# Kernel optimization log

Measured on AMD Instinct MI355X. Metric: run time of the kernel, lower is better.

The kernel has to match this reference:

```python
import jax, jax.numpy as jnp
import numpy as np


def setup_inputs() -> dict:
    key = jax.random.key(0)
    k1, k2 = jax.random.split(key)
    d_feat, n, out_dim = 4096, 8192, 2048
    x = jax.random.normal(k1, (d_feat, n), dtype=jnp.float32)
    Psi = jax.random.normal(k2, (out_dim, n), dtype=jnp.float32)
    return {"x": x, "Psi": Psi}


def reference(x, Psi):
    # Original: out = Psi @ H @ x.T @ x with H = I_n - (1/n) * ones(n, n).
    # Psi @ H subtracts the row-mean of Psi (centering over the sample axis),
    # which is mathematically identical but avoids materializing the n x n H.
    Psi_c = Psi - jnp.mean(Psi, axis=1, keepdims=True)        # [out_dim, n]
    tmp = jnp.einsum('on,dn->od', Psi_c, x)                   # Psi_c @ x.T -> [out_dim, d]
    out = jnp.einsum('od,dn->on', tmp, x)                     # @ x -> [out_dim, n]
    return out
```

## Files before the change

### kernel.cpp

```cpp
#include <hip/hip_runtime.h>
#include <cstdint>
#include <cstddef>


typedef __bf16 bf16x8 __attribute__((ext_vector_type(8)));
typedef float f32x4 __attribute__((ext_vector_type(4)));

__device__ __forceinline__ unsigned short f2bf(float f) {
  unsigned u = __builtin_bit_cast(unsigned, f);
  u += 0x7FFFu + ((u >> 16) & 1u);
  return (unsigned short)(u >> 16);
}

__device__ __forceinline__ void gload_lds16(const void* g, void* l) {
  __builtin_amdgcn_global_load_lds(
      (const __attribute__((address_space(1))) unsigned int*)g,
      (__attribute__((address_space(3))) unsigned int*)l, 16, 0, 0);
}

__device__ __forceinline__ void barrier_nofence() {
  asm volatile("" ::: "memory");
  __builtin_amdgcn_s_barrier();
  asm volatile("" ::: "memory");
}
#define WAIT_LGKM0()                                   \
  do {                                                 \
    asm volatile("s_waitcnt lgkmcnt(0)" ::: "memory"); \
    __builtin_amdgcn_sched_barrier(0);                 \
  } while (0)
#define WAITV(N) asm volatile("s_waitcnt vmcnt(" #N ")" ::: "memory")

__global__ __launch_bounds__(512, 2) void gemm2p(
    const unsigned short* __restrict__ A, const unsigned short* __restrict__ B,
    unsigned short* __restrict__ C, int M, int Nc, int K) {
  constexpr int BM = 128, BN = 256;
  constexpr int APLANE = BM * 64, ABUF = 2 * APLANE;
  constexpr int BPLANE = BN * 64, BBUF = 2 * BPLANE;
  __shared__ __align__(1024) char lds[2 * ABUF + 2 * BBUF];
  char* Al = lds;
  char* Bl = lds + 2 * ABUF;

  const int nwg = gridDim.x * gridDim.y;
  const int wgid = blockIdx.y * gridDim.x + blockIdx.x;
  const int swz = (wgid & 7) * (nwg >> 3) + (wgid >> 3);
  const int bx = swz % gridDim.x, by = swz / gridDim.x;
  const int tileM = by * BM, tileN = bx * BN;

  const int t = threadIdx.x, lane = t & 63, wave = t >> 6;
  const int wm = wave >> 2, wn = wave & 3;
  const int rsel = lane & 15;
  const int cs = (((lane >> 4) ^ (((lane >> 3) & 1) << 1)) << 4);

  const unsigned short* Ag = A + (size_t)tileM * K;
  const unsigned short* Bg = B + (size_t)tileN * K;
  const int cgA = (((t & 3) ^ (((t >> 5) & 1) << 1))) * 8;
  const int NT = K / 64;

  auto stageA = [&](int h, int kt) {
    int b2 = kt & 1;
    int r = h * 64 + ((t >> 2) & 63);
    int kk = t >> 8;
    gload_lds16(Ag + (size_t)r * K + kt * 64 + kk * 32 + cgA,
                Al + b2 * ABUF + kk * APLANE + h * 4096 + (t & 255) * 16);
  };
  auto stageB = [&](int h, int kt) {
    int b2 = kt & 1;
#pragma unroll
    for (int kk = 0; kk < 2; ++kk) {
      int r = h * 128 + (t >> 2);
      gload_lds16(Bg + (size_t)r * K + kt * 64 + kk * 32 + cgA,
                  Bl + b2 * BBUF + kk * BPLANE + h * 8192 + t * 16);
    }
  };

  f32x4 acc[4][4] = {};
  bf16x8 aF[2][2], bFall[4][2];

  stageB(0, 0); stageA(0, 0); stageB(1, 0); stageA(1, 0);
  WAITV(1);
  barrier_nofence();

  for (int kt = 0; kt < NT; ++kt) {
    const char* Ab = Al + (kt & 1) * ABUF;
    const char* Bb = Bl + (kt & 1) * BBUF;
#pragma unroll
    for (int f = 0; f < 2; ++f)
#pragma unroll
      for (int kk = 0; kk < 2; ++kk)
        aF[f][kk] = *(const bf16x8*)(Ab + kk * APLANE +
                                     ((2 * f + wm) * 16 + rsel) * 64 + cs);
#pragma unroll
    for (int g = 0; g < 4; ++g)
#pragma unroll
      for (int kk = 0; kk < 2; ++kk)
        bFall[g][kk] = *(const bf16x8*)(Bb + kk * BPLANE +
                                        ((4 * g + wn) * 16 + rsel) * 64 + cs);
    if (kt + 1 < NT) { stageB(0, kt + 1); stageA(0, kt + 1); }
    barrier_nofence();
    WAIT_LGKM0();
    __builtin_amdgcn_s_setprio(1);
#pragma unroll
    for (int f = 0; f < 2; ++f)
#pragma unroll
      for (int g = 0; g < 4; ++g)
#pragma unroll
        for (int kk = 0; kk < 2; ++kk)
          acc[f][g] = __builtin_amdgcn_mfma_f32_16x16x32_bf16(
              aF[f][kk], bFall[g][kk], acc[f][g], 0, 0, 0);
    __builtin_amdgcn_s_setprio(0);
    if (kt == NT - 1) { WAITV(0); } else { WAITV(3); }
    barrier_nofence();
#pragma unroll
    for (int f = 0; f < 2; ++f)
#pragma unroll
      for (int kk = 0; kk < 2; ++kk)
        aF[f][kk] = *(const bf16x8*)(Ab + kk * APLANE +
                                     ((2 * (f + 2) + wm) * 16 + rsel) * 64 + cs);
    if (kt + 1 < NT) { stageB(1, kt + 1); stageA(1, kt + 1); }
    barrier_nofence();
    WAIT_LGKM0();
    __builtin_amdgcn_s_setprio(1);
#pragma unroll
    for (int f = 0; f < 2; ++f)
#pragma unroll
      for (int g = 0; g < 4; ++g)
#pragma unroll
        for (int kk = 0; kk < 2; ++kk)
          acc[2 + f][g] = __builtin_amdgcn_mfma_f32_16x16x32_bf16(
              aF[f][kk], bFall[g][kk], acc[2 + f][g], 0, 0, 0);
    __builtin_amdgcn_s_setprio(0);
    WAITV(1);
    barrier_nofence();
  }

#pragma unroll
  for (int f = 0; f < 4; ++f) {
    int row0 = tileM + (2 * f + wm) * 16 + ((lane >> 4) << 2);
#pragma unroll
    for (int g = 0; g < 4; ++g) {
      int col = tileN + (4 * g + wn) * 16 + rsel;
#pragma unroll
      for (int r = 0; r < 4; ++r)
        C[(size_t)(row0 + r) * Nc + col] = f2bf(acc[f][g][r]);
    }
  }
}

__global__ __launch_bounds__(512, 2) void gemm4p(
    const unsigned short* __restrict__ A, const unsigned short* __restrict__ B,
    float* __restrict__ C, int M, int Nc, int K) {
  constexpr int BM = 256, BN = 256;
  constexpr int APLANE = BM * 64, ABUF = 2 * APLANE;
  constexpr int BPLANE = BN * 64, BBUF = 2 * BPLANE;
  __shared__ __align__(1024) char lds[2 * ABUF + 2 * BBUF];
  char* Al = lds;
  char* Bl = lds + 2 * ABUF;

  const int nwg = gridDim.x * gridDim.y;
  const int wgid = blockIdx.y * gridDim.x + blockIdx.x;
  const int swz = (wgid & 7) * (nwg >> 3) + (wgid >> 3);
  const int bx = swz % gridDim.x, by = swz / gridDim.x;
  const int tileM = by * BM, tileN = bx * BN;

  const int t = threadIdx.x, lane = t & 63, wave = t >> 6;
  const int wm = wave >> 2, wn = wave & 3;
  const int rsel = lane & 15;
  const int cs = (((lane >> 4) ^ (((lane >> 3) & 1) << 1)) << 4);

  const unsigned short* Ag = A + (size_t)tileM * K;
  const unsigned short* Bg = B + (size_t)tileN * K;
  const int cgA = (((t & 3) ^ (((t >> 5) & 1) << 1))) * 8;
  const int NT = K / 64;

  auto stageA = [&](int h, int kt) {
    int b2 = kt & 1;
#pragma unroll
    for (int kk = 0; kk < 2; ++kk) {
      int r = h * 128 + (t >> 2);
      gload_lds16(Ag + (size_t)r * K + kt * 64 + kk * 32 + cgA,
                  Al + b2 * ABUF + kk * APLANE + h * 8192 + t * 16);
    }
  };
  auto stageB = [&](int h, int kt) {
    int b2 = kt & 1;
#pragma unroll
    for (int kk = 0; kk < 2; ++kk) {
      int r = h * 128 + (t >> 2);
      gload_lds16(Bg + (size_t)r * K + kt * 64 + kk * 32 + cgA,
                  Bl + b2 * BBUF + kk * BPLANE + h * 8192 + t * 16);
    }
  };

  f32x4 acc[8][4] = {};
  bf16x8 aF[4][2], bF0[2][2], bF1[2][2];

  stageA(0, 0); stageB(1, 0); stageA(1, 0); stageB(0, 0);
  stageA(0, 1); stageB(1, 1); stageA(1, 1);
  WAITV(6);
  barrier_nofence();

  for (int kt = 0; kt < NT; ++kt) {
    const char* Ab = Al + (kt & 1) * ABUF;
    const char* Bb = Bl + (kt & 1) * BBUF;
#pragma unroll
    for (int f = 0; f < 4; ++f)
#pragma unroll
      for (int kk = 0; kk < 2; ++kk)
        aF[f][kk] = *(const bf16x8*)(Ab + kk * APLANE +
                                     ((2 * f + wm) * 16 + rsel) * 64 + cs);
#pragma unroll
    for (int g = 0; g < 2; ++g)
#pragma unroll
      for (int kk = 0; kk < 2; ++kk)
        bF0[g][kk] = *(const bf16x8*)(Bb + kk * BPLANE +
                                      ((4 * g + wn) * 16 + rsel) * 64 + cs);
    if (kt + 1 < NT) stageB(0, kt + 1);
    barrier_nofence();
    WAIT_LGKM0();
    __builtin_amdgcn_s_setprio(1);
#pragma unroll
    for (int f = 0; f < 4; ++f)
#pragma unroll
      for (int g = 0; g < 2; ++g)
#pragma unroll
        for (int kk = 0; kk < 2; ++kk)
          acc[f][g] = __builtin_amdgcn_mfma_f32_16x16x32_bf16(
              aF[f][kk], bF0[g][kk], acc[f][g], 0, 0, 0);
    __builtin_amdgcn_s_setprio(0);
    barrier_nofence();
#pragma unroll
    for (int g = 0; g < 2; ++g)
#pragma unroll
      for (int kk = 0; kk < 2; ++kk)
        bF1[g][kk] = *(const bf16x8*)(Bb + kk * BPLANE +
                                      ((4 * (g + 2) + wn) * 16 + rsel) * 64 + cs);
    if (kt + 2 < NT) stageA(0, kt + 2);
    barrier_nofence();
    WAIT_LGKM0();
    __builtin_amdgcn_s_setprio(1);
#pragma unroll
    for (int f = 0; f < 4; ++f)
#pragma unroll
      for (int g = 0; g < 2; ++g)
#pragma unroll
        for (int kk = 0; kk < 2; ++kk)
          acc[f][2 + g] = __builtin_amdgcn_mfma_f32_16x16x32_bf16(
              aF[f][kk], bF1[g][kk], acc[f][2 + g], 0, 0, 0);
    __builtin_amdgcn_s_setprio(0);
    barrier_nofence();
#pragma unroll
    for (int f = 0; f < 4; ++f)
#pragma unroll
      for (int kk = 0; kk < 2; ++kk)
        aF[f][kk] = *(const bf16x8*)(Ab + kk * APLANE +
                                     ((2 * (f + 4) + wm) * 16 + rsel) * 64 + cs);
    if (kt + 2 < NT) stageB(1, kt + 2);
    barrier_nofence();
    WAIT_LGKM0();
    __builtin_amdgcn_s_setprio(1);
#pragma unroll
    for (int f = 0; f < 4; ++f)
#pragma unroll
      for (int g = 0; g < 2; ++g)
#pragma unroll
        for (int kk = 0; kk < 2; ++kk)
          acc[4 + f][2 + g] = __builtin_amdgcn_mfma_f32_16x16x32_bf16(
              aF[f][kk], bF1[g][kk], acc[4 + f][2 + g], 0, 0, 0);
    __builtin_amdgcn_s_setprio(0);
    barrier_nofence();
    if (kt + 2 < NT) stageA(1, kt + 2);
    __builtin_amdgcn_s_setprio(1);
#pragma unroll
    for (int f = 0; f < 4; ++f)
#pragma unroll
      for (int g = 0; g < 2; ++g)
#pragma unroll
        for (int kk = 0; kk < 2; ++kk)
          acc[4 + f][g] = __builtin_amdgcn_mfma_f32_16x16x32_bf16(
              aF[f][kk], bF0[g][kk], acc[4 + f][g], 0, 0, 0);
    __builtin_amdgcn_s_setprio(0);
    if (kt + 2 < NT) { WAITV(6); } else { WAITV(0); }
    barrier_nofence();
  }

#pragma unroll
  for (int f = 0; f < 8; ++f) {
    int row0 = tileM + (2 * f + wm) * 16 + ((lane >> 4) << 2);
#pragma unroll
    for (int g = 0; g < 4; ++g) {
      int col = tileN + (4 * g + wn) * 16 + rsel;
#pragma unroll
      for (int r = 0; r < 4; ++r)
        C[(size_t)(row0 + r) * Nc + col] = acc[f][g][r];
    }
  }
}

__global__ void pre_kernel(const float* __restrict__ x,
                           const float* __restrict__ Psi,
                           unsigned short* __restrict__ xb,
                           unsigned short* __restrict__ xtb,
                           unsigned short* __restrict__ pc, int D, int N) {
  __shared__ unsigned short tileT[64][66];
  __shared__ float red[4];
  const int bid = blockIdx.x, t = threadIdx.x;
  if (bid < 8192) {
    const int n0 = (bid & 127) * 64, d0 = (bid >> 7) * 64;
    const int tx = t & 15, ty = t >> 4;
#pragma unroll
    for (int dy = 0; dy < 4; ++dy) {
      int d = ty + 16 * dy;
      float4 v = *(const float4*)(x + (size_t)(d0 + d) * N + n0 + tx * 4);
      ushort4 o;
      o.x = f2bf(v.x); o.y = f2bf(v.y); o.z = f2bf(v.z); o.w = f2bf(v.w);
      *(ushort4*)(xb + (size_t)(d0 + d) * N + n0 + tx * 4) = o;
      tileT[tx * 4 + 0][d] = o.x;
      tileT[tx * 4 + 1][d] = o.y;
      tileT[tx * 4 + 2][d] = o.z;
      tileT[tx * 4 + 3][d] = o.w;
    }
    __syncthreads();
#pragma unroll
    for (int ny = 0; ny < 4; ++ny) {
      int n = ty + 16 * ny;
      ushort2 a = *(const ushort2*)&tileT[n][tx * 4];
      ushort2 b = *(const ushort2*)&tileT[n][tx * 4 + 2];
      ushort4 o; o.x = a.x; o.y = a.y; o.z = b.x; o.w = b.y;
      *(ushort4*)(xtb + (size_t)(n0 + n) * D + d0 + tx * 4) = o;
    }
  } else {
    const int row = bid - 8192;
    const float4* src = (const float4*)(Psi + (size_t)row * N);
    int n4 = N >> 2;
    float s = 0.f;
    for (int i = t; i < n4; i += blockDim.x) {
      float4 v = src[i];
      s += (v.x + v.y) + (v.z + v.w);
    }
#pragma unroll
    for (int off = 32; off > 0; off >>= 1) s += __shfl_down(s, off);
    if ((t & 63) == 0) red[t >> 6] = s;
    __syncthreads();
    float mean = (red[0] + red[1] + red[2] + red[3]) / (float)N;
    ushort4* dst = (ushort4*)(pc + (size_t)row * N);
    for (int i = t; i < n4; i += blockDim.x) {
      float4 v = src[i];
      ushort4 o;
      o.x = f2bf(v.x - mean);
      o.y = f2bf(v.y - mean);
      o.z = f2bf(v.z - mean);
      o.w = f2bf(v.w - mean);
      dst[i] = o;
    }
  }
}

extern "C" void kernel_launch(void* const* d_in, const int* in_sizes, int n_in,
                              void* d_out, int out_size, void* d_ws,
                              size_t ws_size, hipStream_t stream) {
  const int D = 4096, N = 8192, O = 2048;
  const float* x = (const float*)d_in[0];
  const float* Psi = (const float*)d_in[1];
  float* out = (float*)d_out;

  char* ws = (char*)d_ws;
  unsigned short* xb = (unsigned short*)(ws);
  unsigned short* xtb = (unsigned short*)(ws + ((size_t)64 << 20));
  unsigned short* pc = (unsigned short*)(ws + ((size_t)128 << 20));
  unsigned short* tmpb = (unsigned short*)(ws + ((size_t)160 << 20));

  pre_kernel<<<8192 + O, 256, 0, stream>>>(x, Psi, xb, xtb, pc, D, N);
  gemm2p<<<dim3(D / 256, O / 128), 512, 0, stream>>>(pc, xb, tmpb, O, D, N);
  gemm4p<<<dim3(N / 256, O / 256), 512, 0, stream>>>(tmpb, xtb, out, O, N, D);
}
```

Before: 560.7 us.

## Triple-buffer first GEMM with single barrier per k-step; reuse B fragments in second GEMM

```diff
diff --git a/kernel.cpp b/kernel.cpp
--- a/kernel.cpp
+++ b/kernel.cpp
@@ -30,21 +30,19 @@
   } while (0)
 #define WAITV(N) asm volatile("s_waitcnt vmcnt(" #N ")" ::: "memory")
 
-__global__ __launch_bounds__(512, 2) void gemm2p(
+__global__ __launch_bounds__(512, 2) void gemm_tb(
     const unsigned short* __restrict__ A, const unsigned short* __restrict__ B,
     unsigned short* __restrict__ C, int M, int Nc, int K) {
-  constexpr int BM = 128, BN = 256;
-  constexpr int APLANE = BM * 64, ABUF = 2 * APLANE;
-  constexpr int BPLANE = BN * 64, BBUF = 2 * BPLANE;
-  __shared__ __align__(1024) char lds[2 * ABUF + 2 * BBUF];
-  char* Al = lds;
-  char* Bl = lds + 2 * ABUF;
+  constexpr int TILE = 49152;
+  constexpr int APLANE = 8192;
+  constexpr int BPLANE = 16384;
+  __shared__ __align__(1024) char lds[3 * TILE];
 
   const int nwg = gridDim.x * gridDim.y;
   const int wgid = blockIdx.y * gridDim.x + blockIdx.x;
   const int swz = (wgid & 7) * (nwg >> 3) + (wgid >> 3);
   const int bx = swz % gridDim.x, by = swz / gridDim.x;
-  const int tileM = by * BM, tileN = bx * BN;
+  const int tileM = by * 128, tileN = bx * 256;
 
   const int t = threadIdx.x, lane = t & 63, wave = t >> 6;
   const int wm = wave >> 2, wn = wave & 3;
@@ -56,12 +54,109 @@
   const int cgA = (((t & 3) ^ (((t >> 5) & 1) << 1))) * 8;
   const int NT = K / 64;
 
+  auto stage_tile = [&](int kt) {
+    char* base = lds + (kt % 3) * TILE;
+#pragma unroll
+    for (int h = 0; h < 2; ++h)
+#pragma unroll
+      for (int kk = 0; kk < 2; ++kk) {
+        int r = h * 128 + (t >> 2);
+        gload_lds16(Bg + (size_t)r * K + kt * 64 + kk * 32 + cgA,
+                    base + 16384 + kk * BPLANE + h * 8192 + t * 16);
+      }
+#pragma unroll
+    for (int h = 0; h < 2; ++h) {
+      int r = h * 64 + ((t >> 2) & 63);
+      int kk = t >> 8;
+      gload_lds16(Ag + (size_t)r * K + kt * 64 + kk * 32 + cgA,
+                  base + kk * APLANE + h * 4096 + (t & 255) * 16);
+    }
+  };
+
+  f32x4 acc[4][4] = {};
+  bf16x8 aF[4][2], bF[4][2];
+
+  stage_tile(0);
+  stage_tile(1);
+  WAITV(6);
+  barrier_nofence();
+
+  for (int kt = 0; kt < NT; ++kt) {
+    const char* Ab = lds + (kt % 3) * TILE;
+    const char* Bb = Ab + 16384;
+#pragma unroll
+    for (int f = 0; f < 4; ++f)
+#pragma unroll
+      for (int kk = 0; kk < 2; ++kk)
+        aF[f][kk] = *(const bf16x8*)(Ab + kk * APLANE +
+                                     ((2 * f + wm) * 16 + rsel) * 64 + cs);
+#pragma unroll
+    for (int g = 0; g < 4; ++g)
+#pragma unroll
+      for (int kk = 0; kk < 2; ++kk)
+        bF[g][kk] = *(const bf16x8*)(Bb + kk * BPLANE +
+                                     ((4 * g + wn) * 16 + rsel) * 64 + cs);
+    if (kt + 2 < NT) stage_tile(kt + 2);
+    __builtin_amdgcn_s_setprio(1);
+#pragma unroll
+    for (int f = 0; f < 4; ++f)
+#pragma unroll
+      for (int g = 0; g < 4; ++g)
+#pragma unroll
+        for (int kk = 0; kk < 2; ++kk)
+          acc[f][g] = __builtin_amdgcn_mfma_f32_16x16x32_bf16(
+              aF[f][kk], bF[g][kk], acc[f][g], 0, 0, 0);
+    __builtin_amdgcn_s_setprio(0);
+    if (kt + 2 < NT) { WAITV(6); } else { WAITV(0); }
+    barrier_nofence();
+  }
+
+#pragma unroll
+  for (int f = 0; f < 4; ++f) {
+    int row0 = tileM + (2 * f + wm) * 16 + ((lane >> 4) << 2);
+#pragma unroll
+    for (int g = 0; g < 4; ++g) {
+      int col = tileN + (4 * g + wn) * 16 + rsel;
+#pragma unroll
+      for (int r = 0; r < 4; ++r)
+        C[(size_t)(row0 + r) * Nc + col] = f2bf(acc[f][g][r]);
+    }
+  }
+}
+
+__global__ __launch_bounds__(512, 2) void gemm8p256(
+    const unsigned short* __restrict__ A, const unsigned short* __restrict__ B,
+    float* __restrict__ C, int M, int Nc, int K) {
+  constexpr int APLANE = 256 * 64, ABUF = 2 * APLANE;
+  constexpr int BPLANE = 256 * 64, BBUF = 2 * BPLANE;
+  __shared__ __align__(1024) char lds[2 * ABUF + 2 * BBUF];
+  char* Al = lds;
+  char* Bl = lds + 2 * ABUF;
+
+  const int nwg = gridDim.x * gridDim.y;
+  const int wgid = blockIdx.y * gridDim.x + blockIdx.x;
+  const int swz = (wgid & 7) * (nwg >> 3) + (wgid >> 3);
+  const int bx = swz % gridDim.x, by = swz / gridDim.x;
+  const int tileM = by * 256, tileN = bx * 256;
+
+  const int t = threadIdx.x, lane = t & 63, wave = t >> 6;
+  const int wm = wave >> 2, wn = wave & 3;
+  const int rsel = lane & 15;
+  const int cs = (((lane >> 4) ^ (((lane >> 3) & 1) << 1)) << 4);
+
+  const unsigned short* Ag = A + (size_t)tileM * K;
+  const unsigned short* Bg = B + (size_t)tileN * K;
+  const int cgA = (((t & 3) ^ (((t >> 5) & 1) << 1))) * 8;
+  const int NT = K / 64;
+
   auto stageA = [&](int h, int kt) {
     int b2 = kt & 1;
-    int r = h * 64 + ((t >> 2) & 63);
-    int kk = t >> 8;
-    gload_lds16(Ag + (size_t)r * K + kt * 64 + kk * 32 + cgA,
-                Al + b2 * ABUF + kk * APLANE + h * 4096 + (t & 255) * 16);
+#pragma unroll
+    for (int kk = 0; kk < 2; ++kk) {
+      int r = h * 128 + (t >> 2);
+      gload_lds16(Ag + (size_t)r * K + kt * 64 + kk * 32 + cgA,
+                  Al + b2 * ABUF + kk * APLANE + h * 8192 + t * 16);
+    }
   };
   auto stageB = [&](int h, int kt) {
     int b2 = kt & 1;
@@ -73,126 +168,8 @@
     }
   };
 
-  f32x4 acc[4][4] = {};
-  bf16x8 aF[2][2], bFall[4][2];
-
-  stageB(0, 0); stageA(0, 0); stageB(1, 0); stageA(1, 0);
-  WAITV(1);
-  barrier_nofence();
-
-  for (int kt = 0; kt < NT; ++kt) {
-    const char* Ab = Al + (kt & 1) * ABUF;
-    const char* Bb = Bl + (kt & 1) * BBUF;
-#pragma unroll
-    for (int f = 0; f < 2; ++f)
-#pragma unroll
-      for (int kk = 0; kk < 2; ++kk)
-        aF[f][kk] = *(const bf16x8*)(Ab + kk * APLANE +
-                                     ((2 * f + wm) * 16 + rsel) * 64 + cs);
-#pragma unroll
-    for (int g = 0; g < 4; ++g)
-#pragma unroll
-      for (int kk = 0; kk < 2; ++kk)
-        bFall[g][kk] = *(const bf16x8*)(Bb + kk * BPLANE +
-                                        ((4 * g + wn) * 16 + rsel) * 64 + cs);
-    if (kt + 1 < NT) { stageB(0, kt + 1); stageA(0, kt + 1); }
-    barrier_nofence();
-    WAIT_LGKM0();
-    __builtin_amdgcn_s_setprio(1);
-#pragma unroll
-    for (int f = 0; f < 2; ++f)
-#pragma unroll
-      for (int g = 0; g < 4; ++g)
-#pragma unroll
-        for (int kk = 0; kk < 2; ++kk)
-          acc[f][g] = __builtin_amdgcn_mfma_f32_16x16x32_bf16(
-              aF[f][kk], bFall[g][kk], acc[f][g], 0, 0, 0);
-    __builtin_amdgcn_s_setprio(0);
-    if (kt == NT - 1) { WAITV(0); } else { WAITV(3); }
-    barrier_nofence();
-#pragma unroll
-    for (int f = 0; f < 2; ++f)
-#pragma unroll
-      for (int kk = 0; kk < 2; ++kk)
-        aF[f][kk] = *(const bf16x8*)(Ab + kk * APLANE +
-                                     ((2 * (f + 2) + wm) * 16 + rsel) * 64 + cs);
-    if (kt + 1 < NT) { stageB(1, kt + 1); stageA(1, kt + 1); }
-    barrier_nofence();
-    WAIT_LGKM0();
-    __builtin_amdgcn_s_setprio(1);
-#pragma unroll
-    for (int f = 0; f < 2; ++f)
-#pragma unroll
-      for (int g = 0; g < 4; ++g)
-#pragma unroll
-        for (int kk = 0; kk < 2; ++kk)
-          acc[2 + f][g] = __builtin_amdgcn_mfma_f32_16x16x32_bf16(
-              aF[f][kk], bFall[g][kk], acc[2 + f][g], 0, 0, 0);
-    __builtin_amdgcn_s_setprio(0);
-    WAITV(1);
-    barrier_nofence();
-  }
-
-#pragma unroll
-  for (int f = 0; f < 4; ++f) {
-    int row0 = tileM + (2 * f + wm) * 16 + ((lane >> 4) << 2);
-#pragma unroll
-    for (int g = 0; g < 4; ++g) {
-      int col = tileN + (4 * g + wn) * 16 + rsel;
-#pragma unroll
-      for (int r = 0; r < 4; ++r)
-        C[(size_t)(row0 + r) * Nc + col] = f2bf(acc[f][g][r]);
-    }
-  }
-}
-
-__global__ __launch_bounds__(512, 2) void gemm4p(
-    const unsigned short* __restrict__ A, const unsigned short* __restrict__ B,
-    float* __restrict__ C, int M, int Nc, int K) {
-  constexpr int BM = 256, BN = 256;
-  constexpr int APLANE = BM * 64, ABUF = 2 * APLANE;
-  constexpr int BPLANE = BN * 64, BBUF = 2 * BPLANE;
-  __shared__ __align__(1024) char lds[2 * ABUF + 2 * BBUF];
-  char* Al = lds;
-  char* Bl = lds + 2 * ABUF;
-
-  const int nwg = gridDim.x * gridDim.y;
-  const int wgid = blockIdx.y * gridDim.x + blockIdx.x;
-  const int swz = (wgid & 7) * (nwg >> 3) + (wgid >> 3);
-  const int bx = swz % gridDim.x, by = swz / gridDim.x;
-  const int tileM = by * BM, tileN = bx * BN;
-
-  const int t = threadIdx.x, lane = t & 63, wave = t >> 6;
-  const int wm = wave >> 2, wn = wave & 3;
-  const int rsel = lane & 15;
-  const int cs = (((lane >> 4) ^ (((lane >> 3) & 1) << 1)) << 4);
-
-  const unsigned short* Ag = A + (size_t)tileM * K;
-  const unsigned short* Bg = B + (size_t)tileN * K;
-  const int cgA = (((t & 3) ^ (((t >> 5) & 1) << 1))) * 8;
-  const int NT = K / 64;
-
-  auto stageA = [&](int h, int kt) {
-    int b2 = kt & 1;
-#pragma unroll
-    for (int kk = 0; kk < 2; ++kk) {
-      int r = h * 128 + (t >> 2);
-      gload_lds16(Ag + (size_t)r * K + kt * 64 + kk * 32 + cgA,
-                  Al + b2 * ABUF + kk * APLANE + h * 8192 + t * 16);
-    }
-  };
-  auto stageB = [&](int h, int kt) {
-    int b2 = kt & 1;
-#pragma unroll
-    for (int kk = 0; kk < 2; ++kk) {
-      int r = h * 128 + (t >> 2);
-      gload_lds16(Bg + (size_t)r * K + kt * 64 + kk * 32 + cgA,
-                  Bl + b2 * BBUF + kk * BPLANE + h * 8192 + t * 16);
-    }
-  };
-
   f32x4 acc[8][4] = {};
-  bf16x8 aF[4][2], bF0[2][2], bF1[2][2];
+  bf16x8 aF[4][2], bF[2][2];
 
   stageA(0, 0); stageB(1, 0); stageA(1, 0); stageB(0, 0);
   stageA(0, 1); stageB(1, 1); stageA(1, 1);
@@ -212,8 +189,8 @@
     for (int g = 0; g < 2; ++g)
 #pragma unroll
       for (int kk = 0; kk < 2; ++kk)
-        bF0[g][kk] = *(const bf16x8*)(Bb + kk * BPLANE +
-                                      ((4 * g + wn) * 16 + rsel) * 64 + cs);
+        bF[g][kk] = *(const bf16x8*)(Bb + kk * BPLANE +
+                                     ((4 * g + wn) * 16 + rsel) * 64 + cs);
     if (kt + 1 < NT) stageB(0, kt + 1);
     barrier_nofence();
     WAIT_LGKM0();
@@ -225,15 +202,15 @@
 #pragma unroll
         for (int kk = 0; kk < 2; ++kk)
           acc[f][g] = __builtin_amdgcn_mfma_f32_16x16x32_bf16(
-              aF[f][kk], bF0[g][kk], acc[f][g], 0, 0, 0);
+              aF[f][kk], bF[g][kk], acc[f][g], 0, 0, 0);
     __builtin_amdgcn_s_setprio(0);
     barrier_nofence();
 #pragma unroll
     for (int g = 0; g < 2; ++g)
 #pragma unroll
       for (int kk = 0; kk < 2; ++kk)
-        bF1[g][kk] = *(const bf16x8*)(Bb + kk * BPLANE +
-                                      ((4 * (g + 2) + wn) * 16 + rsel) * 64 + cs);
+        bF[g][kk] = *(const bf16x8*)(Bb + kk * BPLANE +
+                                     ((4 * (g + 2) + wn) * 16 + rsel) * 64 + cs);
     if (kt + 2 < NT) stageA(0, kt + 2);
     barrier_nofence();
     WAIT_LGKM0();
@@ -245,7 +222,7 @@
 #pragma unroll
         for (int kk = 0; kk < 2; ++kk)
           acc[f][2 + g] = __builtin_amdgcn_mfma_f32_16x16x32_bf16(
-              aF[f][kk], bF1[g][kk], acc[f][2 + g], 0, 0, 0);
+              aF[f][kk], bF[g][kk], acc[f][2 + g], 0, 0, 0);
     __builtin_amdgcn_s_setprio(0);
     barrier_nofence();
 #pragma unroll
@@ -265,10 +242,18 @@
 #pragma unroll
         for (int kk = 0; kk < 2; ++kk)
           acc[4 + f][2 + g] = __builtin_amdgcn_mfma_f32_16x16x32_bf16(
-              aF[f][kk], bF1[g][kk], acc[4 + f][2 + g], 0, 0, 0);
-    __builtin_amdgcn_s_setprio(0);
-    barrier_nofence();
+              aF[f][kk], bF[g][kk], acc[4 + f][2 + g], 0, 0, 0);
+    __builtin_amdgcn_s_setprio(0);
+    barrier_nofence();
+#pragma unroll
+    for (int g = 0; g < 2; ++g)
+#pragma unroll
+      for (int kk = 0; kk < 2; ++kk)
+        bF[g][kk] = *(const bf16x8*)(Bb + kk * BPLANE +
+                                     ((4 * g + wn) * 16 + rsel) * 64 + cs);
     if (kt + 2 < NT) stageA(1, kt + 2);
+    barrier_nofence();
+    WAIT_LGKM0();
     __builtin_amdgcn_s_setprio(1);
 #pragma unroll
     for (int f = 0; f < 4; ++f)
@@ -277,7 +262,7 @@
 #pragma unroll
         for (int kk = 0; kk < 2; ++kk)
           acc[4 + f][g] = __builtin_amdgcn_mfma_f32_16x16x32_bf16(
-              aF[f][kk], bF0[g][kk], acc[4 + f][g], 0, 0, 0);
+              aF[f][kk], bF[g][kk], acc[4 + f][g], 0, 0, 0);
     __builtin_amdgcn_s_setprio(0);
     if (kt + 2 < NT) { WAITV(6); } else { WAITV(0); }
     barrier_nofence();
@@ -370,6 +355,6 @@
   unsigned short* tmpb = (unsigned short*)(ws + ((size_t)160 << 20));
 
   pre_kernel<<<8192 + O, 256, 0, stream>>>(x, Psi, xb, xtb, pc, D, N);
-  gemm2p<<<dim3(D / 256, O / 128), 512, 0, stream>>>(pc, xb, tmpb, O, D, N);
-  gemm4p<<<dim3(N / 256, O / 256), 512, 0, stream>>>(tmpb, xtb, out, O, N, D);
-}
+  gemm_tb<<<dim3(D / 256, O / 128), 512, 0, stream>>>(pc, xb, tmpb, O, D, N);
+  gemm8p256<<<dim3(N / 256, O / 256), 512, 0, stream>>>(tmpb, xtb, out, O, N, D);
+}
```

After: 537.9 us. -4.1%, faster.
